# Optimization experiments

Hardware: AMD Instinct MI355X
Metric: run time of the kernel (lower is better)

## Reference

```python
import jax, jax.numpy as jnp
import numpy as np

C = 5          # max within-cluster spike gap (module-level constant in source repo)
DELTA = 0.05   # margin constant (module-level constant in source repo)
B, T, N = 128, 512, 256


def setup_inputs() -> dict:
    key = jax.random.key(0)
    k1, k2, k3 = jax.random.split(key, 3)
    vmem = jax.random.normal(k1, (B, T, N), dtype=jnp.float32) - 1.5
    vlastmem = jax.random.normal(k2, (B, T, N), dtype=jnp.float32)  # unused by the loss math
    labels_t = jax.random.randint(k3, (B, N), 0, 4)
    ratio = jnp.float32(0.5)
    return {"vmem": vmem, "vlastmem": vlastmem, "labels_t": labels_t, "ratio": ratio}


def _per_neuron(v, key):
    """v: [T] membrane trace for one (batch, neuron). Returns (num_cluster, under_term, max_over)."""
    Tn = v.shape[0]
    t = jnp.arange(Tn)
    spike = v >= 0.0
    s = spike.astype(jnp.int32)
    # prefix sums: cs[i] = number of spikes in v[:i]
    cs = jnp.concatenate([jnp.zeros(1, jnp.int32), jnp.cumsum(s)])
    # new cluster starts at t iff spike[t] and no spike in [t-C, t-1]  (gap > C)
    prev_cnt = cs[t] - cs[jnp.clip(t - C, 0, Tn)]
    is_start = spike & (prev_cnt == 0)
    nclu = jnp.sum(is_start.astype(jnp.int32))
    # under-branch mask = union over clusters of [first-C, last+C] = C-dilation of spike train
    dil_cnt = cs[jnp.clip(t + C + 1, 0, Tn)] - cs[jnp.clip(t - C, 0, Tn)]
    mask = dil_cnt > 0

    # per-cluster stats via segmented reductions (cluster id = running count of starts)
    cid = jnp.clip(jnp.cumsum(is_start.astype(jnp.int32)) - 1, 0, Tn - 1)
    counts = jax.ops.segment_sum(s, cid, num_segments=Tn)
    first = jax.ops.segment_min(jnp.where(spike, t, Tn), cid, num_segments=Tn)
    last = jax.ops.segment_max(jnp.where(spike, t, -1), cid, num_segments=Tn)

    # over branch: cluster minimizing (end_idx - beg_idx) == min spike count (first on ties)
    counts_q = jnp.where(t < nclu, counts, Tn + 2)
    ic = jnp.argmin(counts_q)
    over_mask = (t >= first[ic]) & (t <= last[ic])
    max_over = jnp.max(jnp.where(over_mask, v, -jnp.inf))

    # under branch: if unmasked timesteps remain, penalize -max(v[mask==0]);
    # else take v at a (pinned-seed) random spike position
    has_zero = jnp.any(~mask)
    max_unmask = jnp.max(jnp.where(~mask, v, -jnp.inf))
    nsp = cs[-1]
    sorted_pos = jnp.sort(jnp.where(spike, t, Tn))
    r = jax.random.randint(key, (), 0, jnp.maximum(nsp, 1))
    v_rand = v[jnp.clip(sorted_pos[r], 0, Tn - 1)]
    under_term = jnp.where(has_zero, -max_unmask, v_rand)
    return nclu, under_term, max_over


def _forward(vmem, vlastmem, labels_t, ratio):
    Bv, Tv, Nv = vmem.shape
    vflat = jnp.swapaxes(vmem, 1, 2).reshape(Bv * Nv, Tv)   # [B*N, T]
    lflat = labels_t.reshape(Bv * Nv)
    keys = jax.random.split(jax.random.key(42), Bv * Nv)     # pinned seed for the random-spike pick
    nclu, under_term, max_over = jax.vmap(_per_neuron)(vflat, keys)
    ncf = nclu.astype(vmem.dtype)
    margin = DELTA * ratio * ncf
    under = jnp.where(lflat > nclu, under_term + margin, 0.0)
    over = jnp.where(lflat < nclu, max_over + margin, 0.0)
    loss = jnp.sum(under + over)
    spike_output = ncf.reshape(Bv, Nv)
    return loss, spike_output


def reference(vmem, vlastmem, labels_t, ratio):
    return _forward(vmem, vlastmem, labels_t, ratio)
```

## Files before the change

kernel.cpp:

```cpp
#include <hip/hip_runtime.h>
#include <stdint.h>

#define TDIM 512
#define NDIM 256
#define CGAP 5
#define DELTA_C 0.05f
#define NSEG 8
#define SEGT 64
#define BIGI (1 << 28)

typedef unsigned long long u64;
typedef unsigned int u32;


__device__ __forceinline__ int  ctz64(u64 x)   { return x ? __builtin_ctzll(x) : 64; }
__device__ __forceinline__ int  hib64(u64 x)   { return x ? 63 - __builtin_clzll(x) : -1; }
__device__ __forceinline__ u64  below64(int p) { return (p >= 64) ? ~0ull : ((1ull << p) - 1ull); }

extern "C" __global__ void __launch_bounds__(512, 4)
stca_kernel(const float* __restrict__ vmem, const int* __restrict__ labels,
            const float* __restrict__ ratio_p, float* __restrict__ out,
            float* __restrict__ ws) {
  __shared__ u32 sw_lo[NSEG * 64], sw_hi[NSEG * 64];
  __shared__ int s_nclu[NSEG * 64], s_fs[NSEG * 64], s_ls[NSEG * 64];
  __shared__ int s_pc[NSEG * 64], s_pl[NSEG * 64];
  __shared__ int s_sc[NSEG * 64], s_sf[NSEG * 64];
  __shared__ int s_bc[NSEG * 64], s_bf[NSEG * 64], s_bl[NSEG * 64];
  __shared__ int pn_nclu[64], pn_tf[64], pn_tl[64];
  __shared__ float sO[NSEG * 64], sU[NSEG * 64];

  const int lane = threadIdx.x & 63;
  const int seg  = threadIdx.x >> 6;
  const int idx  = threadIdx.x;
  const int blk  = blockIdx.x;
  const int b    = blk >> 2;
  const int n0   = (blk & 3) << 6;
  const int n    = n0 + lane;

  const float* g = vmem + (size_t)b * TDIM * NDIM + n;
  const int t0 = seg * SEGT;

  const float* gp = g + (size_t)t0 * NDIM;
#define LD(i) const float v##i = gp[(i) * NDIM];
  LD(0)  LD(1)  LD(2)  LD(3)  LD(4)  LD(5)  LD(6)  LD(7)
  LD(8)  LD(9)  LD(10) LD(11) LD(12) LD(13) LD(14) LD(15)
  LD(16) LD(17) LD(18) LD(19) LD(20) LD(21) LD(22) LD(23)
  LD(24) LD(25) LD(26) LD(27) LD(28) LD(29) LD(30) LD(31)
  LD(32) LD(33) LD(34) LD(35) LD(36) LD(37) LD(38) LD(39)
  LD(40) LD(41) LD(42) LD(43) LD(44) LD(45) LD(46) LD(47)
  LD(48) LD(49) LD(50) LD(51) LD(52) LD(53) LD(54) LD(55)
  LD(56) LD(57) LD(58) LD(59) LD(60) LD(61) LD(62) LD(63)
#undef LD

#define SB(i) ((v##i >= 0.f) ? (1u << ((i) & 31)) : 0u)
  const u32 blo = SB(0)  | SB(1)  | SB(2)  | SB(3)  | SB(4)  | SB(5)  | SB(6)  | SB(7)
                | SB(8)  | SB(9)  | SB(10) | SB(11) | SB(12) | SB(13) | SB(14) | SB(15)
                | SB(16) | SB(17) | SB(18) | SB(19) | SB(20) | SB(21) | SB(22) | SB(23)
                | SB(24) | SB(25) | SB(26) | SB(27) | SB(28) | SB(29) | SB(30) | SB(31);
  const u32 bhi = SB(32) | SB(33) | SB(34) | SB(35) | SB(36) | SB(37) | SB(38) | SB(39)
                | SB(40) | SB(41) | SB(42) | SB(43) | SB(44) | SB(45) | SB(46) | SB(47)
                | SB(48) | SB(49) | SB(50) | SB(51) | SB(52) | SB(53) | SB(54) | SB(55)
                | SB(56) | SB(57) | SB(58) | SB(59) | SB(60) | SB(61) | SB(62) | SB(63);
#undef SB
  const u64 s = (u64)blo | ((u64)bhi << 32);

  u64 w5 = (s << 1) | (s << 2);
  w5 |= (s << 3) | (s << 4) | (s << 5);
  const u64 starts = s & ~w5;
  const int nclu = __popcll(starts);
  const int fs_l = ctz64(s);
  const int ls_l = hib64(s);
  const u64 st2 = starts & (starts - 1);
  const int p2  = ctz64(st2);
  const u64 pm  = s & below64(p2);
  const int pcnt  = __popcll(pm);
  const int pls_l = hib64(pm);
  const int plast = (nclu >= 1) ? hib64(starts) : 0;
  const int scnt  = __popcll(s >> plast);
  int bcnt = BIGI, bfs_l = 0, bls_l = 0;
  u64 rem = st2;
  while ((rem & (rem - 1)) != 0ull) {
    const int p   = ctz64(rem);
    const u64 rem2 = rem & (rem - 1);
    const int pnx = ctz64(rem2);
    const u64 m   = s & below64(pnx) & ~below64(p);
    const int cnt = __popcll(m);
    if (cnt < bcnt) { bcnt = cnt; bfs_l = p; bls_l = hib64(m); }
    rem = rem2;
  }

  sw_lo[idx] = (u32)s;  sw_hi[idx] = (u32)(s >> 32);
  s_nclu[idx] = nclu;
  s_fs[idx] = (nclu >= 1) ? (t0 + fs_l) : BIGI;
  s_ls[idx] = t0 + ls_l;
  s_pc[idx] = pcnt;  s_pl[idx] = t0 + pls_l;
  s_sc[idx] = scnt;  s_sf[idx] = t0 + plast;
  s_bc[idx] = bcnt;  s_bf[idx] = t0 + bfs_l;  s_bl[idx] = t0 + bls_l;
  __syncthreads();

  const u64 sL = (seg > 0)
      ? ((u64)sw_lo[idx - 64] | ((u64)sw_hi[idx - 64] << 32)) : 0ull;
  const u64 sR = (seg < NSEG - 1)
      ? ((u64)sw_lo[idx + 64] | ((u64)sw_hi[idx + 64] << 32)) : 0ull;
  u64 D = s;
  D |= (s << 1) | (sL >> 63);
  D |= (s << 2) | (sL >> 62);
  D |= (s << 3) | (sL >> 61);
  D |= (s << 4) | (sL >> 60);
  D |= (s << 5) | (sL >> 59);
  D |= (s >> 1) | (sR << 63);
  D |= (s >> 2) | (sR << 62);
  D |= (s >> 3) | (sR << 61);
  D |= (s >> 4) | (sR << 60);
  D |= (s >> 5) | (sR << 59);

  int a_nclu = 0;
  if (seg == 0) {
    int a_fs = BIGI, a_ls = 0;
    int a_pcnt = 0, a_pls = 0, a_scnt = 0, a_sfs = 0;
    int a_bcnt = BIGI, a_bfs = 0, a_bls = 0;
    for (int sg = 0; sg < NSEG; ++sg) {
      const int j = (sg << 6) + lane;
      const int r_nclu = s_nclu[j];
      if (r_nclu == 0) continue;
      const int r_fs = s_fs[j], r_ls = s_ls[j];
      const int r_pcnt = s_pc[j], r_pls = s_pl[j];
      const int r_scnt = s_sc[j], r_sfs = s_sf[j];
      const int r_bcnt = s_bc[j], r_bfs = s_bf[j], r_bl = s_bl[j];
      if (a_nclu == 0) {
        a_nclu = r_nclu; a_fs = r_fs; a_ls = r_ls;
        a_pcnt = r_pcnt; a_pls = r_pls; a_scnt = r_scnt; a_sfs = r_sfs;
        a_bcnt = r_bcnt; a_bfs = r_bfs; a_bls = r_bl;
        continue;
      }
      if (r_fs - a_ls <= CGAP) {
        const int Bc = a_scnt + r_pcnt, Bfs = a_sfs, Bls = r_pls;
        int nb = a_bcnt, nbf = a_bfs, nbl = a_bls;
        if (a_nclu >= 2 && r_nclu >= 2 && Bc < nb) { nb = Bc; nbf = Bfs; nbl = Bls; }
        if (r_bcnt < nb) { nb = r_bcnt; nbf = r_bfs; nbl = r_bl; }
        if (a_nclu == 1) { a_pcnt = Bc; a_pls = Bls; }
        if (r_nclu == 1) { a_scnt = Bc; a_sfs = Bfs; }
        else             { a_scnt = r_scnt; a_sfs = r_sfs; }
        a_bcnt = nb; a_bfs = nbf; a_bls = nbl;
        a_nclu += r_nclu - 1;
        a_ls = r_ls;
      } else {
        int nb = a_bcnt, nbf = a_bfs, nbl = a_bls;
        if (a_nclu >= 2 && a_scnt < nb) { nb = a_scnt; nbf = a_sfs; nbl = a_ls; }
        if (r_nclu >= 2 && r_pcnt < nb) { nb = r_pcnt; nbf = r_fs;  nbl = r_pls; }
        if (r_bcnt < nb) { nb = r_bcnt; nbf = r_bfs; nbl = r_bl; }
        a_bcnt = nb; a_bfs = nbf; a_bls = nbl;
        a_scnt = r_scnt; a_sfs = r_sfs;
        a_nclu += r_nclu;
        a_ls = r_ls;
      }
    }
    int tf = a_fs, tl = a_pls, bc = a_pcnt;
    if (a_nclu >= 2) {
      if (a_bcnt < bc) { bc = a_bcnt; tf = a_bfs; tl = a_bls; }
      if (a_scnt < bc) { bc = a_scnt; tf = a_sfs; tl = a_ls; }
    }
    pn_nclu[lane] = a_nclu; pn_tf[lane] = tf; pn_tl[lane] = tl;
    out[1 + b * NDIM + n] = (float)a_nclu;
  }
  __syncthreads();

  const int  label  = labels[b * NDIM + n];
  const int  f_nclu = pn_nclu[lane];
  const int  tf = pn_tf[lane], tl = pn_tl[lane];
  const bool needO = label < f_nclu;
  const bool needU = label > f_nclu;
  int lo = tf - t0; lo = lo < 0 ? 0 : (lo > 64 ? 64 : lo);
  int hi = tl - t0 + 1; hi = hi < 0 ? 0 : (hi > 64 ? 64 : hi);
  const u64 R  = needO ? (below64(hi) & ~below64(lo)) : 0ull;
  const u64 Dm = needU ? ~D : 0ull;
  float mO = -INFINITY, mU = -INFINITY;
#define MO(i) mO = ((R >> (i)) & 1ull) ? fmaxf(mO, v##i) : mO;
  MO(0)  MO(1)  MO(2)  MO(3)  MO(4)  MO(5)  MO(6)  MO(7)
  MO(8)  MO(9)  MO(10) MO(11) MO(12) MO(13) MO(14) MO(15)
  MO(16) MO(17) MO(18) MO(19) MO(20) MO(21) MO(22) MO(23)
  MO(24) MO(25) MO(26) MO(27) MO(28) MO(29) MO(30) MO(31)
  MO(32) MO(33) MO(34) MO(35) MO(36) MO(37) MO(38) MO(39)
  MO(40) MO(41) MO(42) MO(43) MO(44) MO(45) MO(46) MO(47)
  MO(48) MO(49) MO(50) MO(51) MO(52) MO(53) MO(54) MO(55)
  MO(56) MO(57) MO(58) MO(59) MO(60) MO(61) MO(62) MO(63)
#undef MO
  if (__any(Dm != 0ull)) {
#define MU(i) mU = ((Dm >> (i)) & 1ull) ? fmaxf(mU, v##i) : mU;
    MU(0)  MU(1)  MU(2)  MU(3)  MU(4)  MU(5)  MU(6)  MU(7)
    MU(8)  MU(9)  MU(10) MU(11) MU(12) MU(13) MU(14) MU(15)
    MU(16) MU(17) MU(18) MU(19) MU(20) MU(21) MU(22) MU(23)
    MU(24) MU(25) MU(26) MU(27) MU(28) MU(29) MU(30) MU(31)
    MU(32) MU(33) MU(34) MU(35) MU(36) MU(37) MU(38) MU(39)
    MU(40) MU(41) MU(42) MU(43) MU(44) MU(45) MU(46) MU(47)
    MU(48) MU(49) MU(50) MU(51) MU(52) MU(53) MU(54) MU(55)
    MU(56) MU(57) MU(58) MU(59) MU(60) MU(61) MU(62) MU(63)
#undef MU
  }
  sO[idx] = mO; sU[idx] = mU;
  __syncthreads();

  if (seg != 0) return;

  float mo = sO[lane], mu = sU[lane];
#pragma unroll
  for (int sg = 1; sg < NSEG; ++sg) {
    mo = fmaxf(mo, sO[(sg << 6) + lane]);
    mu = fmaxf(mu, sU[(sg << 6) + lane]);
  }
  const float ratio  = ratio_p[0];
  const float ncf    = (float)a_nclu;
  const float margin = DELTA_C * ratio * ncf;
  const float under_term = (mu > -INFINITY) ? (-mu) : 0.0f;
  const float under = (label > a_nclu) ? (under_term + margin) : 0.0f;
  const float over  = (label < a_nclu) ? (mo + margin) : 0.0f;

  float sum = under + over;
#pragma unroll
  for (int off = 32; off > 0; off >>= 1) sum += __shfl_down(sum, off);
  if (lane == 0) ws[blk] = sum;
}

extern "C" __global__ void __launch_bounds__(64, 1)
stca_reduce(const float* __restrict__ ws, float* __restrict__ out) {
  const int lane = threadIdx.x;
  float s = 0.0f;
#pragma unroll
  for (int i = 0; i < 8; ++i) s += ws[lane + (i << 6)];
#pragma unroll
  for (int off = 32; off > 0; off >>= 1) s += __shfl_down(s, off);
  if (lane == 0) out[0] = s;
}

extern "C" void kernel_launch(void* const* d_in, const int* in_sizes, int n_in,
                              void* d_out, int out_size, void* d_ws,
                              size_t ws_size, hipStream_t stream) {
  const float* vmem   = (const float*)d_in[0];
  const int*   labels = (const int*)d_in[2];
  const float* ratio  = (const float*)d_in[3];
  float* out = (float*)d_out;
  float* ws  = (float*)d_ws;

  dim3 grid(512);
  dim3 block(512);
  hipLaunchKernelGGL(stca_kernel, grid, block, 0, stream, vmem, labels, ratio,
                     out, ws);
  hipLaunchKernelGGL(stca_reduce, dim3(1), dim3(64), 0, stream, ws, out);
}
```

Baseline: 146.7 us.

## Pack per-segment cluster stats into three words and merge redundantly in all waves

Each segment's cluster summary (counts and offsets) is now bit-packed into three 32-bit shared words instead of eleven int arrays. Every wave reads all eight segments and runs the merge itself, so the second block barrier and the broadcast through shared memory are gone. The label load is hoisted to the top, and launch bounds drop from 4 to 2 blocks per CU. The cost is eight times more merge work, and the 8-bit fields assume per-segment counts stay below 255.

```diff
diff --git a/kernel.cpp b/kernel.cpp
--- a/kernel.cpp
+++ b/kernel.cpp
@@ -17,16 +17,12 @@
 __device__ __forceinline__ int  hib64(u64 x)   { return x ? 63 - __builtin_clzll(x) : -1; }
 __device__ __forceinline__ u64  below64(int p) { return (p >= 64) ? ~0ull : ((1ull << p) - 1ull); }
 
-extern "C" __global__ void __launch_bounds__(512, 4)
+extern "C" __global__ void __launch_bounds__(512, 2)
 stca_kernel(const float* __restrict__ vmem, const int* __restrict__ labels,
             const float* __restrict__ ratio_p, float* __restrict__ out,
             float* __restrict__ ws) {
   __shared__ u32 sw_lo[NSEG * 64], sw_hi[NSEG * 64];
-  __shared__ int s_nclu[NSEG * 64], s_fs[NSEG * 64], s_ls[NSEG * 64];
-  __shared__ int s_pc[NSEG * 64], s_pl[NSEG * 64];
-  __shared__ int s_sc[NSEG * 64], s_sf[NSEG * 64];
-  __shared__ int s_bc[NSEG * 64], s_bf[NSEG * 64], s_bl[NSEG * 64];
-  __shared__ int pn_nclu[64], pn_tf[64], pn_tl[64];
+  __shared__ u32 sp0[NSEG * 64], sp1[NSEG * 64], sp2[NSEG * 64];
   __shared__ float sO[NSEG * 64], sU[NSEG * 64];
 
   const int lane = threadIdx.x & 63;
@@ -39,6 +35,7 @@
 
   const float* g = vmem + (size_t)b * TDIM * NDIM + n;
   const int t0 = seg * SEGT;
+  const int label = labels[b * NDIM + n];
 
   const float* gp = g + (size_t)t0 * NDIM;
 #define LD(i) const float v##i = gp[(i) * NDIM];
@@ -77,7 +74,7 @@
   const int pls_l = hib64(pm);
   const int plast = (nclu >= 1) ? hib64(starts) : 0;
   const int scnt  = __popcll(s >> plast);
-  int bcnt = BIGI, bfs_l = 0, bls_l = 0;
+  int bcnt = 255, bfs_l = 0, bls_l = 0;
   u64 rem = st2;
   while ((rem & (rem - 1)) != 0ull) {
     const int p   = ctz64(rem);
@@ -89,13 +86,12 @@
     rem = rem2;
   }
 
-  sw_lo[idx] = (u32)s;  sw_hi[idx] = (u32)(s >> 32);
-  s_nclu[idx] = nclu;
-  s_fs[idx] = (nclu >= 1) ? (t0 + fs_l) : BIGI;
-  s_ls[idx] = t0 + ls_l;
-  s_pc[idx] = pcnt;  s_pl[idx] = t0 + pls_l;
-  s_sc[idx] = scnt;  s_sf[idx] = t0 + plast;
-  s_bc[idx] = bcnt;  s_bf[idx] = t0 + bfs_l;  s_bl[idx] = t0 + bls_l;
+  sw_lo[idx] = blo;  sw_hi[idx] = bhi;
+  sp0[idx] = (u32)nclu | ((u32)(fs_l & 255) << 8) | ((u32)(ls_l & 255) << 16)
+           | ((u32)pcnt << 24);
+  sp1[idx] = (u32)(pls_l & 255) | ((u32)scnt << 8) | ((u32)(plast & 255) << 16)
+           | ((u32)bcnt << 24);
+  sp2[idx] = (u32)(bfs_l & 255) | ((u32)(bls_l & 255) << 8);
   __syncthreads();
 
   const u64 sL = (seg > 0)
@@ -114,26 +110,31 @@
   D |= (s >> 4) | (sR << 60);
   D |= (s >> 5) | (sR << 59);
 
-  int a_nclu = 0;
-  if (seg == 0) {
-    int a_fs = BIGI, a_ls = 0;
-    int a_pcnt = 0, a_pls = 0, a_scnt = 0, a_sfs = 0;
-    int a_bcnt = BIGI, a_bfs = 0, a_bls = 0;
-    for (int sg = 0; sg < NSEG; ++sg) {
-      const int j = (sg << 6) + lane;
-      const int r_nclu = s_nclu[j];
-      if (r_nclu == 0) continue;
-      const int r_fs = s_fs[j], r_ls = s_ls[j];
-      const int r_pcnt = s_pc[j], r_pls = s_pl[j];
-      const int r_scnt = s_sc[j], r_sfs = s_sf[j];
-      const int r_bcnt = s_bc[j], r_bfs = s_bf[j], r_bl = s_bl[j];
+  int a_nclu = 0, a_fs = BIGI, a_ls = 0;
+  int a_pcnt = 0, a_pls = 0, a_scnt = 0, a_sfs = 0;
+  int a_bcnt = BIGI, a_bfs = 0, a_bls = 0;
+#pragma unroll
+  for (int sg = 0; sg < NSEG; ++sg) {
+    const int j = (sg << 6) + lane;
+    const u32 a0 = sp0[j], a1 = sp1[j], a2 = sp2[j];
+    const int r_nclu = (int)(a0 & 255u);
+    if (r_nclu != 0) {
+      const int t0s = sg << 6;
+      const int r_fs   = t0s + (int)((a0 >> 8) & 255u);
+      const int r_ls   = t0s + (int)((a0 >> 16) & 255u);
+      const int r_pcnt = (int)((a0 >> 24) & 255u);
+      const int r_pls  = t0s + (int)(a1 & 255u);
+      const int r_scnt = (int)((a1 >> 8) & 255u);
+      const int r_sfs  = t0s + (int)((a1 >> 16) & 255u);
+      const int rb_raw = (int)((a1 >> 24) & 255u);
+      const int r_bcnt = (rb_raw == 255) ? BIGI : rb_raw;
+      const int r_bfs  = t0s + (int)(a2 & 255u);
+      const int r_bl   = t0s + (int)((a2 >> 8) & 255u);
       if (a_nclu == 0) {
         a_nclu = r_nclu; a_fs = r_fs; a_ls = r_ls;
         a_pcnt = r_pcnt; a_pls = r_pls; a_scnt = r_scnt; a_sfs = r_sfs;
         a_bcnt = r_bcnt; a_bfs = r_bfs; a_bls = r_bl;
-        continue;
-      }
-      if (r_fs - a_ls <= CGAP) {
+      } else if (r_fs - a_ls <= CGAP) {
         const int Bc = a_scnt + r_pcnt, Bfs = a_sfs, Bls = r_pls;
         int nb = a_bcnt, nbf = a_bfs, nbl = a_bls;
         if (a_nclu >= 2 && r_nclu >= 2 && Bc < nb) { nb = Bc; nbf = Bfs; nbl = Bls; }
@@ -155,21 +156,16 @@
         a_ls = r_ls;
       }
     }
-    int tf = a_fs, tl = a_pls, bc = a_pcnt;
-    if (a_nclu >= 2) {
-      if (a_bcnt < bc) { bc = a_bcnt; tf = a_bfs; tl = a_bls; }
-      if (a_scnt < bc) { bc = a_scnt; tf = a_sfs; tl = a_ls; }
-    }
-    pn_nclu[lane] = a_nclu; pn_tf[lane] = tf; pn_tl[lane] = tl;
-    out[1 + b * NDIM + n] = (float)a_nclu;
-  }
-  __syncthreads();
-
-  const int  label  = labels[b * NDIM + n];
-  const int  f_nclu = pn_nclu[lane];
-  const int  tf = pn_tf[lane], tl = pn_tl[lane];
-  const bool needO = label < f_nclu;
-  const bool needU = label > f_nclu;
+  }
+  int tf = a_fs, tl = a_pls, bc = a_pcnt;
+  if (a_nclu >= 2) {
+    if (a_bcnt < bc) { bc = a_bcnt; tf = a_bfs; tl = a_bls; }
+    if (a_scnt < bc) { bc = a_scnt; tf = a_sfs; tl = a_ls; }
+  }
+  if (seg == 0) out[1 + b * NDIM + n] = (float)a_nclu;
+
+  const bool needO = label < a_nclu;
+  const bool needU = label > a_nclu;
   int lo = tf - t0; lo = lo < 0 ? 0 : (lo > 64 ? 64 : lo);
   int hi = tl - t0 + 1; hi = hi < 0 ? 0 : (hi > 64 ? 64 : hi);
   const u64 R  = needO ? (below64(hi) & ~below64(lo)) : 0ull;
```

New measurement: 145.3 us. About the same (-0.9%).
